# Optimization experiments

Measured on AMD Instinct MI355X. Metric: run time of the kernel, lower is better.

The kernel has to match this reference:

```python
import jax, jax.numpy as jnp
import numpy as np

N, F, D, K = 4096, 128, 64, 2  # nodes, in_dim, out_dim, hops


def setup_inputs() -> dict:
    key = jax.random.key(0)
    k_x, k_a, k_e, k_w = jax.random.split(key, 4)
    X = jax.random.normal(k_x, (N, F), jnp.float32)
    # K+1 non-negative dense adjacency/distance matrices (stacked list)
    A = jax.random.uniform(k_a, (K + 1, N, N), jnp.float32)
    # Dense(out_dim, use_bias=False) weights, glorot-like scale
    W_emb = jax.random.normal(k_e, (F, D), jnp.float32) / np.sqrt(F)
    W_hops = jax.random.normal(k_w, (K + 1, F, D), jnp.float32) / np.sqrt(F)
    alpha = jnp.float32(0.1)
    return {"X": X, "A": A, "W_emb": W_emb, "W_hops": W_hops, "alpha": alpha}


def reference(X, A, W_emb, W_hops, alpha):
    # learned embeddings E = Dense(X)  -> [N, D]
    E = X @ W_emb
    # shared low-rank update alpha * E @ E^T  -> [N, N]
    low_rank = alpha * (E @ E.T)
    # per-hop kernel projections Dense_k(X)  -> [K+1, N, D]
    XW = jnp.einsum('nf,kfd->knd', X, W_hops)
    out = jnp.zeros((N, D), X.dtype)
    for k in range(A.shape[0]):  # fixed small K+1 hops
        A_hat = A[k] + low_rank                       # [N, N]
        deg = jnp.sum(A_hat, axis=1)                  # row sums
        d = jnp.power(deg, -0.5)                      # D^{-1/2}
        # D^{-1/2} A_hat D^{-1/2} via broadcast scaling (same math as diag matmuls)
        A_norm = d[:, None] * A_hat * d[None, :]
        out = out + A_norm @ XW[k]
    return jax.nn.relu(out)
```

## Files before the change

### kernel.cpp

```cpp
#include <hip/hip_runtime.h>
#include <math.h>

#define N_ 4096
#define F_ 128
#define D_ 64
#define KH_ 3
#define ZS_ 8
#define KC_ (N_ / ZS_)

#define OFF_E      0
#define OFF_XW     (N_*D_)
#define OFF_SE     (OFF_XW + KH_*N_*D_)
#define OFF_T      (OFF_SE + D_)
#define OFF_DVEC   (OFF_T + KH_*D_*D_)
#define OFF_YT     (OFF_DVEC + KH_*N_)
#define OFF_AYP    (OFF_YT + KH_*D_*N_/2)

typedef __attribute__((ext_vector_type(8))) short bf16x8;
typedef __attribute__((ext_vector_type(4))) float f32x4;

static __device__ __forceinline__ unsigned short f2bf(float f) {
  union { float f; unsigned u; } v; v.f = f;
  unsigned r = (v.u + 0x7fffu + ((v.u >> 16) & 1u)) >> 16;
  return (unsigned short)r;
}

__global__ __launch_bounds__(256) void proj_kernel(
    const float* __restrict__ X, const float* __restrict__ W_emb,
    const float* __restrict__ W_hops, float* __restrict__ ws)
{
  __shared__ __align__(16) float sXT[32][68];
  __shared__ __align__(16) float sW[32][68];
  const int t = threadIdx.x;
  const int m = blockIdx.y;
  const int row0 = blockIdx.x * 64;
  const float* W = (m == 0) ? W_emb : (W_hops + (size_t)(m - 1) * F_ * D_);
  float* out = (m == 0) ? (ws + OFF_E) : (ws + OFF_XW + (size_t)(m - 1) * N_ * D_);
  const int tx = t & 15, ty = t >> 4;
  const int d0 = tx * 4, i0 = ty * 4;
  float acc[4][4] = {};
  for (int fc = 0; fc < F_; fc += 32) {
    {
      int i_l = t >> 3;
      int f_l = (t & 7) * 4;
      for (int r = 0; r < 2; ++r) {
        int i = i_l + r * 32;
        float4 v = *(const float4*)(X + (size_t)(row0 + i) * F_ + fc + f_l);
        sXT[f_l + 0][i] = v.x; sXT[f_l + 1][i] = v.y;
        sXT[f_l + 2][i] = v.z; sXT[f_l + 3][i] = v.w;
      }
      int f2 = t >> 4;
      int d  = (t & 15) * 4;
      for (int r = 0; r < 2; ++r) {
        int f = f2 + r * 16;
        *(float4*)&sW[f][d] = *(const float4*)(W + (size_t)(fc + f) * D_ + d);
      }
    }
    __syncthreads();
#pragma unroll 8
    for (int f = 0; f < 32; ++f) {
      float a[4], b[4];
      *(float4*)a = *(const float4*)&sXT[f][i0];
      *(float4*)b = *(const float4*)&sW[f][d0];
      for (int x = 0; x < 4; ++x)
        for (int y = 0; y < 4; ++y)
          acc[x][y] += a[x] * b[y];
    }
    __syncthreads();
  }
  for (int x = 0; x < 4; ++x)
    *(float4*)(out + (size_t)(row0 + i0 + x) * D_ + d0) = *(float4*)acc[x];
}

__global__ __launch_bounds__(256) void colsum_kernel(
    const float* __restrict__ E, float* __restrict__ S)
{
  int t = threadIdx.x;
  int d = t & 63;
  int sub = t >> 6;
  int i0 = blockIdx.x * 64;
  float acc = 0.f;
  for (int i = i0 + sub; i < i0 + 64; i += 4)
    acc += E[(size_t)i * D_ + d];
  atomicAdd(&S[d], acc);
}

__global__ __launch_bounds__(256) void degree_kernel(
    const float* __restrict__ A, const float* __restrict__ E,
    const float* __restrict__ S, const float* __restrict__ alpha_p,
    float* __restrict__ dvec)
{
  int lane = threadIdx.x & 63;
  int wave = threadIdx.x >> 6;
  int row = blockIdx.x * 4 + wave;
  int i = row & (N_ - 1);
  const float4* Ar = (const float4*)(A + (size_t)row * N_);
  float s = 0.f;
#pragma unroll
  for (int it = 0; it < 16; ++it) {
    float4 v = Ar[lane + it * 64];
    s += (v.x + v.y) + (v.z + v.w);
  }
  float alpha = *alpha_p;
  s += alpha * E[(size_t)i * D_ + lane] * S[lane];
#pragma unroll
  for (int off = 32; off > 0; off >>= 1)
    s += __shfl_xor(s, off);
  if (lane == 0) dvec[row] = 1.0f / sqrtf(s);
}

__global__ __launch_bounds__(256) void yprep_kernel(float* __restrict__ ws)
{
  const int k = blockIdx.y;
  const int j0 = blockIdx.x * 64;
  const float* XWk = ws + OFF_XW + (size_t)k * N_ * D_;
  const float* dk  = ws + OFF_DVEC + (size_t)k * N_;
  unsigned short* Ytk = (unsigned short*)(ws + OFF_YT) + (size_t)k * D_ * N_;
  __shared__ float sT[64][65];
  int t = threadIdx.x;
  {
    int j = t >> 2;
    int c0 = (t & 3) * 16;
    float dv = dk[j0 + j];
    for (int r = 0; r < 4; ++r) {
      float4 v = *(const float4*)(XWk + (size_t)(j0 + j) * D_ + c0 + 4 * r);
      sT[c0 + 4 * r + 0][j] = v.x * dv;
      sT[c0 + 4 * r + 1][j] = v.y * dv;
      sT[c0 + 4 * r + 2][j] = v.z * dv;
      sT[c0 + 4 * r + 3][j] = v.w * dv;
    }
  }
  __syncthreads();
  {
    int n = t >> 2;
    int jq = (t & 3) * 16;
    __align__(16) unsigned short buf[16];
#pragma unroll
    for (int i = 0; i < 16; ++i) buf[i] = f2bf(sT[n][jq + i]);
    uint4* dst = (uint4*)(Ytk + (size_t)n * N_ + j0 + jq);
    dst[0] = *(uint4*)&buf[0];
    dst[1] = *(uint4*)&buf[8];
  }
}

__global__ __launch_bounds__(256) void tmat_kernel(
    const float* __restrict__ ws, float* __restrict__ T)
{
  const float* E   = ws + OFF_E;
  const float* XWk = ws + OFF_XW + (size_t)blockIdx.y * N_ * D_;
  const float* dk  = ws + OFF_DVEC + (size_t)blockIdx.y * N_;
  __shared__ __align__(16) float sE[32][68];
  __shared__ __align__(16) float sY[32][68];
  int t = threadIdx.x;
  int tx = t & 15, ty = t >> 4;
  int d0 = tx * 4, c0 = ty * 4;
  float acc[4][4] = {};
  int base0 = blockIdx.x * 128;
  for (int sub = 0; sub < 4; ++sub) {
    int base = base0 + sub * 32;
    {
      int i_l = t >> 3;
      int c   = (t & 7) * 4;
      float dv = dk[base + i_l];
      for (int r = 0; r < 2; ++r) {
        int col = c + r * 32;
        *(float4*)&sE[i_l][col] = *(const float4*)(E + (size_t)(base + i_l) * D_ + col);
        float4 y = *(const float4*)(XWk + (size_t)(base + i_l) * D_ + col);
        y.x *= dv; y.y *= dv; y.z *= dv; y.w *= dv;
        *(float4*)&sY[i_l][col] = y;
      }
    }
    __syncthreads();
#pragma unroll 8
    for (int i = 0; i < 32; ++i) {
      float c4[4], y4[4];
      *(float4*)c4 = *(const float4*)&sE[i][c0];
      *(float4*)y4 = *(const float4*)&sY[i][d0];
      for (int a = 0; a < 4; ++a)
        for (int b = 0; b < 4; ++b)
          acc[a][b] += c4[a] * y4[b];
    }
    __syncthreads();
  }
  float* Tk = T + (size_t)blockIdx.y * D_ * D_;
  for (int a = 0; a < 4; ++a)
    for (int b = 0; b < 4; ++b)
      atomicAdd(&Tk[(c0 + a) * D_ + d0 + b], acc[a][b]);
}

__global__ __launch_bounds__(256) void agemm_kernel(
    const float* __restrict__ A, const float* __restrict__ ws,
    float* __restrict__ AYp)
{
  const int k = blockIdx.y;
  const int row0 = blockIdx.x * 64;
  const int kz0 = blockIdx.z * KC_;
  const float* Ak = A + ((size_t)k << 24);
  const unsigned short* Ytk = (const unsigned short*)(ws + OFF_YT) + (size_t)k * D_ * N_;

  __shared__ __align__(16) unsigned short sA[64][72];
  __shared__ __align__(16) unsigned short sY[64][72];

  const int t = threadIdx.x;
  const int lane = t & 63;
  const int w = t >> 6;
  const int m = lane & 15;
  const int q = lane >> 4;

  f32x4 acc[4];
#pragma unroll
  for (int i = 0; i < 4; ++i) acc[i] = (f32x4){0.f, 0.f, 0.f, 0.f};

  const int ar  = t >> 2;
  const int akq = (t & 3) * 16;

  for (int kt = 0; kt < KC_; kt += 64) {
    {
      const float* gA = Ak + (size_t)(row0 + ar) * N_ + kz0 + kt + akq;
#pragma unroll
      for (int r = 0; r < 4; ++r) {
        float4 v = *(const float4*)(gA + 4 * r);
        ushort4 u;
        u.x = f2bf(v.x); u.y = f2bf(v.y); u.z = f2bf(v.z); u.w = f2bf(v.w);
        *(ushort4*)&sA[ar][akq + 4 * r] = u;
      }
      const uint4* gY = (const uint4*)(Ytk + (size_t)ar * N_ + kz0 + kt + akq);
      *(uint4*)&sY[ar][akq + 0] = gY[0];
      *(uint4*)&sY[ar][akq + 8] = gY[1];
    }
    __syncthreads();
    const int mrow = w * 16 + m;
#pragma unroll
    for (int s = 0; s < 2; ++s) {
      bf16x8 af = *(const bf16x8*)&sA[mrow][s * 32 + q * 8];
#pragma unroll
      for (int nt = 0; nt < 4; ++nt) {
        bf16x8 bfv = *(const bf16x8*)&sY[nt * 16 + m][s * 32 + q * 8];
        acc[nt] = __builtin_amdgcn_mfma_f32_16x16x32_bf16(af, bfv, acc[nt], 0, 0, 0);
      }
    }
    __syncthreads();
  }
  float* outp = AYp + (((size_t)blockIdx.z * KH_ + k) * N_ + row0 + w * 16) * D_;
#pragma unroll
  for (int nt = 0; nt < 4; ++nt)
#pragma unroll
    for (int r = 0; r < 4; ++r)
      outp[(size_t)(q * 4 + r) * D_ + nt * 16 + m] = acc[nt][r];
}

__global__ __launch_bounds__(256) void epilogue_kernel(
    const float* __restrict__ ws, const float* __restrict__ alpha_p,
    float* __restrict__ out)
{
  int g = blockIdx.x * 256 + threadIdx.x;
  int i = g >> 6, d = g & 63;
  const float* E    = ws + OFF_E;
  const float* T    = ws + OFF_T;
  const float* dvec = ws + OFF_DVEC;
  const float* AYp  = ws + OFF_AYP;
  float alpha = *alpha_p;
  float s = 0.f;
  for (int k = 0; k < KH_; ++k) {
    float ay = 0.f;
#pragma unroll
    for (int jc = 0; jc < ZS_; ++jc)
      ay += AYp[(((size_t)jc * KH_ + k) * N_ + i) * D_ + d];
    float lr = 0.f;
    const float* Tk = T + k * D_ * D_;
#pragma unroll 16
    for (int c = 0; c < D_; ++c)
      lr += E[(size_t)i * D_ + c] * Tk[c * D_ + d];
    s += dvec[k * N_ + i] * (ay + alpha * lr);
  }
  out[g] = fmaxf(s, 0.f);
}

extern "C" void kernel_launch(void* const* d_in, const int* in_sizes, int n_in,
                              void* d_out, int out_size, void* d_ws, size_t ws_size,
                              hipStream_t stream) {
  const float* X      = (const float*)d_in[0];
  const float* A      = (const float*)d_in[1];
  const float* W_emb  = (const float*)d_in[2];
  const float* W_hops = (const float*)d_in[3];
  const float* alpha_p= (const float*)d_in[4];
  float* out = (float*)d_out;
  float* ws  = (float*)d_ws;

  hipMemsetAsync(ws + OFF_SE, 0, (D_ + KH_ * D_ * D_) * sizeof(float), stream);

  proj_kernel<<<dim3(N_ / 64, 4), 256, 0, stream>>>(X, W_emb, W_hops, ws);
  colsum_kernel<<<dim3(N_ / 64), 256, 0, stream>>>(ws + OFF_E, ws + OFF_SE);
  degree_kernel<<<dim3(KH_ * N_ / 4), 256, 0, stream>>>(A, ws + OFF_E, ws + OFF_SE,
                                                        alpha_p, ws + OFF_DVEC);
  yprep_kernel<<<dim3(N_ / 64, KH_), 256, 0, stream>>>(ws);
  tmat_kernel<<<dim3(32, KH_), 256, 0, stream>>>(ws, ws + OFF_T);
  agemm_kernel<<<dim3(N_ / 64, KH_, ZS_), 256, 0, stream>>>(A, ws, ws + OFF_AYP);
  epilogue_kernel<<<dim3(N_ * D_ / 256), 256, 0, stream>>>(ws, alpha_p, out);
}
```

Before: 371.3 us.

## Load MFMA operands directly from global memory, drop LDS staging and barriers

The A-times-Y GEMM kernel no longer stages tiles in shared memory with two barriers per step. Each lane now loads its own A fragment (fp32, converted to bf16) and its Y fragments straight from global memory into MFMA operands, with the loop unrolled by 4. Block order is also reversed so the last-written hop and rows are read first, which may hit data still in cache from the previous kernel. The cost is that the Y loads, which are shared by the four waves, are now fetched separately by each wave through L1/L2 instead of once into LDS, and each lane's global access is a strided 32-byte load.

```diff
diff --git a/kernel.cpp b/kernel.cpp
--- a/kernel.cpp
+++ b/kernel.cpp
@@ -192,14 +192,11 @@
     const float* __restrict__ A, const float* __restrict__ ws,
     float* __restrict__ AYp)
 {
-  const int k = blockIdx.y;
-  const int row0 = blockIdx.x * 64;
+  const int k = KH_ - 1 - blockIdx.y;
+  const int row0 = (gridDim.x - 1 - blockIdx.x) * 64;
   const int kz0 = blockIdx.z * KC_;
   const float* Ak = A + ((size_t)k << 24);
   const unsigned short* Ytk = (const unsigned short*)(ws + OFF_YT) + (size_t)k * D_ * N_;
-
-  __shared__ __align__(16) unsigned short sA[64][72];
-  __shared__ __align__(16) unsigned short sY[64][72];
 
   const int t = threadIdx.x;
   const int lane = t & 63;
@@ -211,35 +208,23 @@
 #pragma unroll
   for (int i = 0; i < 4; ++i) acc[i] = (f32x4){0.f, 0.f, 0.f, 0.f};
 
-  const int ar  = t >> 2;
-  const int akq = (t & 3) * 16;
-
-  for (int kt = 0; kt < KC_; kt += 64) {
-    {
-      const float* gA = Ak + (size_t)(row0 + ar) * N_ + kz0 + kt + akq;
-#pragma unroll
-      for (int r = 0; r < 4; ++r) {
-        float4 v = *(const float4*)(gA + 4 * r);
-        ushort4 u;
-        u.x = f2bf(v.x); u.y = f2bf(v.y); u.z = f2bf(v.z); u.w = f2bf(v.w);
-        *(ushort4*)&sA[ar][akq + 4 * r] = u;
-      }
-      const uint4* gY = (const uint4*)(Ytk + (size_t)ar * N_ + kz0 + kt + akq);
-      *(uint4*)&sY[ar][akq + 0] = gY[0];
-      *(uint4*)&sY[ar][akq + 8] = gY[1];
-    }
-    __syncthreads();
-    const int mrow = w * 16 + m;
-#pragma unroll
-    for (int s = 0; s < 2; ++s) {
-      bf16x8 af = *(const bf16x8*)&sA[mrow][s * 32 + q * 8];
-#pragma unroll
-      for (int nt = 0; nt < 4; ++nt) {
-        bf16x8 bfv = *(const bf16x8*)&sY[nt * 16 + m][s * 32 + q * 8];
-        acc[nt] = __builtin_amdgcn_mfma_f32_16x16x32_bf16(af, bfv, acc[nt], 0, 0, 0);
-      }
-    }
-    __syncthreads();
+  const float* aRow = Ak + (size_t)(row0 + w * 16 + m) * N_ + kz0 + q * 8;
+  const unsigned short* yBase = Ytk + kz0 + q * 8;
+
+#pragma unroll 4
+  for (int kt = 0; kt < KC_; kt += 32) {
+    float4 a0 = *(const float4*)(aRow + kt);
+    float4 a1 = *(const float4*)(aRow + kt + 4);
+    bf16x8 af;
+    af[0] = (short)f2bf(a0.x); af[1] = (short)f2bf(a0.y);
+    af[2] = (short)f2bf(a0.z); af[3] = (short)f2bf(a0.w);
+    af[4] = (short)f2bf(a1.x); af[5] = (short)f2bf(a1.y);
+    af[6] = (short)f2bf(a1.z); af[7] = (short)f2bf(a1.w);
+#pragma unroll
+    for (int nt = 0; nt < 4; ++nt) {
+      bf16x8 bfv = *(const bf16x8*)(yBase + (size_t)(nt * 16 + m) * N_ + kt);
+      acc[nt] = __builtin_amdgcn_mfma_f32_16x16x32_bf16(af, bfv, acc[nt], 0, 0, 0);
+    }
   }
   float* outp = AYp + (((size_t)blockIdx.z * KH_ + k) * N_ + row0 + w * 16) * D_;
 #pragma unroll
```

Measured after the change: 403.8 us. 1.09x slower.
